# Kernel tuning notes

Hardware: AMD Instinct MI355X
Metric: run time of the kernel (lower is better)

## Reference

```python
import jax, jax.numpy as jnp
import numpy as np

B, S, E, H, F = 4, 2048, 1024, 16, 4096
D = E // H
EPS = 1e-5


def setup_inputs() -> dict:
    key = jax.random.key(0)
    ks = jax.random.split(key, 12)
    sc_e = 1.0 / np.sqrt(E)
    sc_f = 1.0 / np.sqrt(F)
    inp = {
        'x': jax.random.normal(ks[0], (B, S, E), jnp.float32),
        'mask': jnp.tril(jnp.ones((S, S), jnp.int32))[None, None],  # causal [1,1,S,S]
        'ln1_g': jnp.ones((E,), jnp.float32),
        'ln1_b': jnp.zeros((E,), jnp.float32),
        'Wq': jax.random.normal(ks[1], (E, E), jnp.float32) * sc_e,
        'bq': jnp.zeros((E,), jnp.float32),
        'Wk': jax.random.normal(ks[2], (E, E), jnp.float32) * sc_e,
        'bk': jnp.zeros((E,), jnp.float32),
        'Wv': jax.random.normal(ks[3], (E, E), jnp.float32) * sc_e,
        'bv': jnp.zeros((E,), jnp.float32),
        'Wo': jax.random.normal(ks[4], (E, E), jnp.float32) * sc_e,
        'bo': jnp.zeros((E,), jnp.float32),
        'ln2_g': jnp.ones((E,), jnp.float32),
        'ln2_b': jnp.zeros((E,), jnp.float32),
        'W1': jax.random.normal(ks[5], (F, E), jnp.float32) * sc_e,
        'b1': jnp.zeros((F,), jnp.float32),
        'W2': jax.random.normal(ks[6], (E, F), jnp.float32) * sc_f,
        'b2': jnp.zeros((E,), jnp.float32),
    }
    return inp


def _ln(x, g, b):
    m = jnp.mean(x, axis=-1, keepdims=True)
    v = jnp.mean(jnp.square(x - m), axis=-1, keepdims=True)
    return (x - m) * jax.lax.rsqrt(v + EPS) * g + b


def _attn(h, mask, Wq, bq, Wk, bk, Wv, bv, Wo, bo):
    b, s, _ = h.shape
    q = (h @ Wq.T + bq).reshape(b, s, H, D)
    k = (h @ Wk.T + bk).reshape(b, s, H, D)
    v = (h @ Wv.T + bv).reshape(b, s, H, D)
    scores = jnp.einsum('bqhd,bkhd->bhqk', q, k) / np.sqrt(D)
    scores = jnp.where(mask == 0, -jnp.inf, scores)
    w = jax.nn.softmax(scores, axis=-1)
    ctx = jnp.einsum('bhqk,bkhd->bqhd', w, v).reshape(b, s, E)
    return ctx @ Wo.T + bo


def reference(x, mask, ln1_g, ln1_b, Wq, bq, Wk, bk, Wv, bv, Wo, bo,
              ln2_g, ln2_b, W1, b1, W2, b2):
    x = x + _attn(_ln(x, ln1_g, ln1_b), mask, Wq, bq, Wk, bk, Wv, bv, Wo, bo)
    h = _ln(x, ln2_g, ln2_b)
    ffn = jax.nn.gelu(h @ W1.T + b1, approximate=False) @ W2.T + b2
    return x + ffn
```

## Files before the change

kernel.cpp:

```cpp
#include <hip/hip_runtime.h>
#include <cstdint>
#include <cstddef>

#define E_DIM 1024
#define F_DIM 4096
#define S_LEN 2048
#define NB    4
#define NH    16
#define HD    64
#define MROWS 8192

typedef __bf16 bf16x8 __attribute__((ext_vector_type(8)));
typedef float  f32x4  __attribute__((ext_vector_type(4)));

struct alignas(16) f4 { float x, y, z, w; };
__device__ __forceinline__ f4 ld4(const float* p){ return *(const f4*)p; }

__device__ __forceinline__ unsigned short f2bf(float f){
  union { float f; unsigned int u; } c; c.f = f;
  unsigned int u = c.u;
  return (unsigned short)((u + 0x7FFFu + ((u >> 16) & 1u)) >> 16);
}

__global__ void cvt_kernel(const float* __restrict__ in, unsigned short* __restrict__ out,
                           int n, float scale){
  int i = (blockIdx.x * 256 + threadIdx.x) * 4;
  if (i >= n) return;
  f4 f = ld4(in + i);
  ushort4 o;
  o.x = f2bf(f.x * scale); o.y = f2bf(f.y * scale);
  o.z = f2bf(f.z * scale); o.w = f2bf(f.w * scale);
  *(ushort4*)(out + i) = o;
}

__global__ void bias_cat(const float* __restrict__ bq, const float* __restrict__ bk,
                         const float* __restrict__ bv, float* __restrict__ out, float qsc){
  int i = blockIdx.x * 256 + threadIdx.x;
  if (i >= 3 * E_DIM) return;
  float v = (i < E_DIM) ? bq[i] * qsc : (i < 2 * E_DIM ? bk[i - E_DIM] : bv[i - 2 * E_DIM]);
  out[i] = v;
}

__global__ __launch_bounds__(256) void ln_kernel(const float* __restrict__ in,
                                                 const float* __restrict__ g,
                                                 const float* __restrict__ b,
                                                 unsigned short* __restrict__ out){
  const int row = blockIdx.x;
  const int t = threadIdx.x;
  const float* xr = in + (size_t)row * E_DIM;
  f4 xv = ld4(xr + t * 4);
  float s  = xv.x + xv.y + xv.z + xv.w;
  float ss = xv.x*xv.x + xv.y*xv.y + xv.z*xv.z + xv.w*xv.w;
  #pragma unroll
  for (int o = 1; o < 64; o <<= 1){ s += __shfl_xor(s, o); ss += __shfl_xor(ss, o); }
  __shared__ float sa[4], sb[4];
  if ((t & 63) == 0){ sa[t >> 6] = s; sb[t >> 6] = ss; }
  __syncthreads();
  s  = sa[0] + sa[1] + sa[2] + sa[3];
  ss = sb[0] + sb[1] + sb[2] + sb[3];
  const float mean = s * (1.0f / E_DIM);
  const float var  = ss * (1.0f / E_DIM) - mean * mean;
  const float rstd = rsqrtf(var + 1e-5f);
  f4 gv = ld4(g + t * 4);
  f4 bv = ld4(b + t * 4);
  ushort4 o;
  o.x = f2bf((xv.x - mean) * rstd * gv.x + bv.x);
  o.y = f2bf((xv.y - mean) * rstd * gv.y + bv.y);
  o.z = f2bf((xv.z - mean) * rstd * gv.z + bv.z);
  o.w = f2bf((xv.w - mean) * rstd * gv.w + bv.w);
  *(ushort4*)(out + (size_t)row * E_DIM + t * 4) = o;
}

__device__ __forceinline__ void async_cp16(const unsigned short* g, unsigned short* l){
  __builtin_amdgcn_global_load_lds((const __attribute__((address_space(1))) unsigned int*)g,
                                   (__attribute__((address_space(3)))       unsigned int*)l,
                                   16, 0, 0);
}

template<int EPI>
__global__ __launch_bounds__(256) void gemm_bt(const unsigned short* __restrict__ A,
                                               const unsigned short* __restrict__ W,
                                               const float* __restrict__ bias,
                                               const float* __restrict__ res,
                                               void* __restrict__ outp,
                                               int M, int N, int K){
  __shared__ unsigned short As[128 * 64];
  __shared__ unsigned short Bs[128 * 64];
  const int bn = blockIdx.x, bm = blockIdx.y;
  const int tid = threadIdx.x;
  const int wv = tid >> 6, lane = tid & 63;
  const int lr = lane & 15, qd = lane >> 4;
  const int wm = (wv >> 1) * 64, wn = (wv & 1) * 64;

  f32x4 acc[4][4];
  #pragma unroll
  for (int mt = 0; mt < 4; ++mt)
    #pragma unroll
    for (int nt = 0; nt < 4; ++nt)
      acc[mt][nt] = f32x4{0.f, 0.f, 0.f, 0.f};

  int soff[4];
  int srow[4];
  #pragma unroll
  for (int it = 0; it < 4; ++it){
    const int cc = tid + it * 256;
    srow[it] = cc >> 3;
    soff[it] = (((cc & 7) ^ (srow[it] & 7))) * 8;
  }
  const unsigned short* Abase = A + (size_t)(bm * 128) * K;
  const unsigned short* Wbase = W + (size_t)(bn * 128) * K;

  for (int k0 = 0; k0 < K; k0 += 64){
    __syncthreads();
    #pragma unroll
    for (int it = 0; it < 4; ++it){
      async_cp16(Abase + (size_t)srow[it] * K + k0 + soff[it], &As[(tid + it * 256) * 8]);
      async_cp16(Wbase + (size_t)srow[it] * K + k0 + soff[it], &Bs[(tid + it * 256) * 8]);
    }
    __builtin_amdgcn_s_waitcnt(0);
    __syncthreads();

    #pragma unroll
    for (int kk = 0; kk < 2; ++kk){
      bf16x8 af[4], bf[4];
      #pragma unroll
      for (int mt = 0; mt < 4; ++mt){
        const int fr = wm + mt * 16 + lr;
        af[mt] = *(const bf16x8*)&As[fr * 64 + (((kk * 4 + qd) ^ (fr & 7))) * 8];
      }
      #pragma unroll
      for (int nt = 0; nt < 4; ++nt){
        const int fr = wn + nt * 16 + lr;
        bf[nt] = *(const bf16x8*)&Bs[fr * 64 + (((kk * 4 + qd) ^ (fr & 7))) * 8];
      }
      #pragma unroll
      for (int mt = 0; mt < 4; ++mt)
        #pragma unroll
        for (int nt = 0; nt < 4; ++nt)
          acc[mt][nt] = __builtin_amdgcn_mfma_f32_16x16x32_bf16(af[mt], bf[nt], acc[mt][nt], 0, 0, 0);
    }
  }

  #pragma unroll
  for (int mt = 0; mt < 4; ++mt){
    #pragma unroll
    for (int r = 0; r < 4; ++r){
      const int gm = bm * 128 + wm + mt * 16 + qd * 4 + r;
      const size_t rowoff = (size_t)gm * N;
      #pragma unroll
      for (int nt = 0; nt < 4; ++nt){
        const int gn = bn * 128 + wn + nt * 16 + lr;
        float v = acc[mt][nt][r] + bias[gn];
        if constexpr (EPI == 1) v = 0.5f * v * (1.0f + erff(v * 0.70710678118654752f));
        if constexpr (EPI == 2) ((float*)outp)[rowoff + gn] = v + res[rowoff + gn];
        else                    ((unsigned short*)outp)[rowoff + gn] = f2bf(v);
      }
    }
  }
}

__global__ __launch_bounds__(256) void vtrans(const unsigned short* __restrict__ QKV,
                                              unsigned short* __restrict__ Vt){
  __shared__ unsigned short Ts[64 * 66];
  const int st = blockIdx.x;
  const int h = blockIdx.y, b = blockIdx.z;
  const int tid = threadIdx.x;
  const size_t srcbase = (size_t)(b * S_LEN + st * 64) * 3072 + 2 * E_DIM + h * HD;
  #pragma unroll
  for (int it = 0; it < 4; ++it){
    const int ch = tid + it * 256;
    const int row = ch >> 4, c4 = (ch & 15) * 4;
    *(ushort4*)&Ts[row * 66 + c4] = *(const ushort4*)(QKV + srcbase + (size_t)row * 3072 + c4);
  }
  __syncthreads();
  const size_t dstbase = (size_t)((b * NH + h) * HD) * S_LEN + st * 64;
  #pragma unroll
  for (int it = 0; it < 4; ++it){
    const int ch = tid + it * 256;
    const int d = ch >> 4, t4 = (ch & 15) * 4;
    ushort4 o;
    o.x = Ts[(t4 + 0) * 66 + d];
    o.y = Ts[(t4 + 1) * 66 + d];
    o.z = Ts[(t4 + 2) * 66 + d];
    o.w = Ts[(t4 + 3) * 66 + d];
    *(ushort4*)&Vt[dstbase + (size_t)d * S_LEN + t4] = o;
  }
}

#define AST 72
__global__ __launch_bounds__(256) void attn_mfma(const unsigned short* __restrict__ QKV,
                                                 const unsigned short* __restrict__ Vt,
                                                 unsigned short* __restrict__ Om){
  __shared__ unsigned short Ks[64 * AST];
  __shared__ unsigned short Vs[64 * AST];
  __shared__ unsigned short Ps[64 * AST];
  const int pairi = blockIdx.x;
  const int h = blockIdx.y, b = blockIdx.z;
  const int tid = threadIdx.x;
  const int w = tid >> 6, lane = tid & 63;
  const int lr = lane & 15, qd = lane >> 4;
  const size_t row0 = (size_t)b * S_LEN;
  const int qcol = h * HD;
  const int kcol = E_DIM + h * HD;
  const unsigned short* Vtb = Vt + (size_t)((b * NH + h) * HD) * S_LEN;

  bf16x8 ones;
  #pragma unroll
  for (int j = 0; j < 8; ++j) ones[j] = (__bf16)1.0f;

  for (int ph = 0; ph < 2; ++ph){
    const int qb_t = ph ? (31 - pairi) : pairi;
    const int q0 = qb_t * 64 + w * 16;

    bf16x8 qf[2];
    #pragma unroll
    for (int kk = 0; kk < 2; ++kk)
      qf[kk] = *(const bf16x8*)(QKV + (row0 + q0 + lr) * 3072 + qcol + kk * 32 + qd * 8);

    f32x4 accd[4];
    #pragma unroll
    for (int dt = 0; dt < 4; ++dt) accd[dt] = f32x4{0.f, 0.f, 0.f, 0.f};
    f32x4 lacc = f32x4{0.f, 0.f, 0.f, 0.f};

    for (int kt = 0; kt <= qb_t; ++kt){
      __syncthreads();
      #pragma unroll
      for (int it = 0; it < 2; ++it){
        const int ch = tid + it * 256;
        const int r_ = ch >> 3, c8 = (ch & 7) * 8;
        *(uint4*)&Ks[r_ * AST + c8] = *(const uint4*)(QKV + (row0 + kt * 64 + r_) * 3072 + kcol + c8);
        *(uint4*)&Vs[r_ * AST + c8] = *(const uint4*)(Vtb + (size_t)r_ * S_LEN + kt * 64 + c8);
      }
      __syncthreads();

      f32x4 s[4];
      #pragma unroll
      for (int nt = 0; nt < 4; ++nt) s[nt] = f32x4{0.f, 0.f, 0.f, 0.f};
      #pragma unroll
      for (int kk = 0; kk < 2; ++kk){
        bf16x8 kf[4];
        #pragma unroll
        for (int nt = 0; nt < 4; ++nt)
          kf[nt] = *(const bf16x8*)&Ks[(nt * 16 + lr) * AST + kk * 32 + qd * 8];
        #pragma unroll
        for (int nt = 0; nt < 4; ++nt)
          s[nt] = __builtin_amdgcn_mfma_f32_16x16x32_bf16(qf[kk], kf[nt], s[nt], 0, 0, 0);
      }
      if (kt == qb_t){
        #pragma unroll
        for (int nt = 0; nt < 4; ++nt)
          #pragma unroll
          for (int r = 0; r < 4; ++r){
            const int q  = q0 + qd * 4 + r;
            const int ky = kt * 64 + nt * 16 + lr;
            if (ky > q) s[nt][r] = -3e38f;
          }
      }
      #pragma unroll
      for (int nt = 0; nt < 4; ++nt)
        #pragma unroll
        for (int r = 0; r < 4; ++r){
          union { float f; unsigned u; } cc;
          cc.f = exp2f(s[nt][r]);
          Ps[(w * 16 + qd * 4 + r) * AST + nt * 16 + lr] = (unsigned short)((cc.u + 0x8000u) >> 16);
        }
      __builtin_amdgcn_s_waitcnt(0xc07f);
      #pragma unroll
      for (int kk = 0; kk < 2; ++kk){
        bf16x8 pf = *(const bf16x8*)&Ps[(w * 16 + lr) * AST + kk * 32 + qd * 8];
        bf16x8 vf[4];
        #pragma unroll
        for (int dt = 0; dt < 4; ++dt)
          vf[dt] = *(const bf16x8*)&Vs[(dt * 16 + lr) * AST + kk * 32 + qd * 8];
        #pragma unroll
        for (int dt = 0; dt < 4; ++dt)
          accd[dt] = __builtin_amdgcn_mfma_f32_16x16x32_bf16(pf, vf[dt], accd[dt], 0, 0, 0);
        lacc = __builtin_amdgcn_mfma_f32_16x16x32_bf16(pf, ones, lacc, 0, 0, 0);
      }
    }

    #pragma unroll
    for (int r = 0; r < 4; ++r){
      const float inv = 1.0f / lacc[r];
      const size_t ro = (row0 + q0 + qd * 4 + r) * E_DIM + qcol;
      #pragma unroll
      for (int dt = 0; dt < 4; ++dt)
        Om[ro + dt * 16 + lr] = f2bf(accd[dt][r] * inv);
    }
  }
}

extern "C" void kernel_launch(void* const* d_in, const int* in_sizes, int n_in,
                              void* d_out, int out_size, void* d_ws, size_t ws_size,
                              hipStream_t stream){
  const float* x    = (const float*)d_in[0];
  const float* ln1g = (const float*)d_in[2];
  const float* ln1b = (const float*)d_in[3];
  const float* Wq   = (const float*)d_in[4];
  const float* bq   = (const float*)d_in[5];
  const float* Wk   = (const float*)d_in[6];
  const float* bk   = (const float*)d_in[7];
  const float* Wv   = (const float*)d_in[8];
  const float* bv   = (const float*)d_in[9];
  const float* Wo   = (const float*)d_in[10];
  const float* bo   = (const float*)d_in[11];
  const float* ln2g = (const float*)d_in[12];
  const float* ln2b = (const float*)d_in[13];
  const float* W1   = (const float*)d_in[14];
  const float* b1   = (const float*)d_in[15];
  const float* W2   = (const float*)d_in[16];
  const float* b2   = (const float*)d_in[17];

  char* ws = (char*)d_ws;
  const size_t MB = 1024 * 1024;
  unsigned short* Wqkv_b = (unsigned short*)(ws + 0 * MB);
  unsigned short* Wo_b   = (unsigned short*)(ws + 6 * MB);
  unsigned short* W1_b   = (unsigned short*)(ws + 8 * MB);
  unsigned short* W2_b   = (unsigned short*)(ws + 16 * MB);
  unsigned short* qkvb   = (unsigned short*)(ws + 24 * MB);
  float*          bqkv   = (float*)(ws + 72 * MB);
  unsigned short* Vt_g   = (unsigned short*)(ws + 72 * MB);
  unsigned short* lnb    = (unsigned short*)(ws + 88 * MB);
  float*          xres   = (float*)(ws + 104 * MB);
  unsigned short* ffn1   = (unsigned short*)(ws + 24 * MB);
  unsigned short* ctxb   = lnb;

  const float QSC = 0.125f * 1.4426950408889634f;

  cvt_kernel<<<1024, 256, 0, stream>>>(Wq, Wqkv_b,                   E_DIM * E_DIM, QSC);
  cvt_kernel<<<1024, 256, 0, stream>>>(Wk, Wqkv_b + E_DIM * E_DIM,   E_DIM * E_DIM, 1.0f);
  cvt_kernel<<<1024, 256, 0, stream>>>(Wv, Wqkv_b + 2 * E_DIM * E_DIM, E_DIM * E_DIM, 1.0f);
  cvt_kernel<<<1024, 256, 0, stream>>>(Wo, Wo_b, E_DIM * E_DIM, 1.0f);
  cvt_kernel<<<4096, 256, 0, stream>>>(W1, W1_b, F_DIM * E_DIM, 1.0f);
  cvt_kernel<<<4096, 256, 0, stream>>>(W2, W2_b, F_DIM * E_DIM, 1.0f);
  bias_cat<<<12, 256, 0, stream>>>(bq, bk, bv, bqkv, QSC);

  ln_kernel<<<MROWS, 256, 0, stream>>>(x, ln1g, ln1b, lnb);

  gemm_bt<0><<<dim3(3 * E_DIM / 128, MROWS / 128), 256, 0, stream>>>(
      lnb, Wqkv_b, bqkv, nullptr, qkvb, MROWS, 3 * E_DIM, E_DIM);

  vtrans<<<dim3(S_LEN / 64, NH, NB), 256, 0, stream>>>(qkvb, Vt_g);

  attn_mfma<<<dim3(16, NH, NB), 256, 0, stream>>>(qkvb, Vt_g, ctxb);

  gemm_bt<2><<<dim3(E_DIM / 128, MROWS / 128), 256, 0, stream>>>(
      ctxb, Wo_b, bo, x, xres, MROWS, E_DIM, E_DIM);

  ln_kernel<<<MROWS, 256, 0, stream>>>(xres, ln2g, ln2b, lnb);

  gemm_bt<1><<<dim3(F_DIM / 128, MROWS / 128), 256, 0, stream>>>(
      lnb, W1_b, b1, nullptr, ffn1, MROWS, F_DIM, E_DIM);

  gemm_bt<2><<<dim3(E_DIM / 128, MROWS / 128), 256, 0, stream>>>(
      ffn1, W2_b, b2, xres, (float*)d_out, MROWS, E_DIM, F_DIM);
}
```

Measured before the change: 577.7 us.

## Add 256x256-tile 8-wave pipelined GEMM for QKV and FFN1 projections

Adds a new GEMM kernel with 256x256 output tiles, 512 threads, double-buffered async global-to-LDS copies with XOR swizzling, and interleaved quarter-tile MFMA phases with barriers and setprio. It is used for the QKV and FFN-up GEMMs in place of the 128x128 kernel, aiming to raise arithmetic intensity per LDS byte and overlap loads with MFMA work. The costs are larger LDS use (128KB per block), many barriers per K step, fewer blocks (grid of 384/512 tiles), and reliance on manual vmcnt waits being correct.

```diff
diff --git a/kernel.cpp b/kernel.cpp
--- a/kernel.cpp
+++ b/kernel.cpp
@@ -157,6 +157,143 @@
       }
     }
   }
+}
+
+#define VMW4() asm volatile("s_waitcnt vmcnt(4)" ::: "memory")
+#define VMW0() asm volatile("s_waitcnt vmcnt(0)" ::: "memory")
+#define BAR()  __builtin_amdgcn_s_barrier()
+
+template<int EPI>
+__global__ __launch_bounds__(512, 2) void gemm256(const unsigned short* __restrict__ A,
+                                                  const unsigned short* __restrict__ W,
+                                                  const float* __restrict__ bias,
+                                                  unsigned short* __restrict__ outp,
+                                                  int M, int N, int K){
+  __shared__ unsigned short lds[2][2][256 * 64];
+  const int bn = blockIdx.x, bm = blockIdx.y;
+  const int tid = threadIdx.x;
+  const int lane = tid & 63;
+  const int wv = tid >> 6;
+  const int lr = lane & 15, qd = lane >> 4;
+  const int wm = wv >> 2, wn = wv & 3;
+  const int NT = K >> 6;
+
+  f32x4 acc[2][2][4][2];
+  #pragma unroll
+  for (int a = 0; a < 2; ++a)
+    #pragma unroll
+    for (int b = 0; b < 2; ++b)
+      #pragma unroll
+      for (int c = 0; c < 4; ++c)
+        #pragma unroll
+        for (int d = 0; d < 2; ++d)
+          acc[a][b][c][d] = f32x4{0.f, 0.f, 0.f, 0.f};
+
+  const int srow = tid >> 3;
+  const int scol = ((tid & 7) ^ (srow & 7)) * 8;
+  const unsigned short* Ab = A + (size_t)(bm * 256 + srow) * K + scol;
+  const unsigned short* Wb = W + (size_t)(bn * 256 + srow) * K + scol;
+
+#define STAGE_A(bufi, h, kt) do{ \
+    async_cp16(Ab + (size_t)((h)*128     ) * K + (size_t)(kt) * 64, &lds[bufi][0][((h)*128     ) * 64 + tid * 8]); \
+    async_cp16(Ab + (size_t)((h)*128 + 64) * K + (size_t)(kt) * 64, &lds[bufi][0][((h)*128 + 64) * 64 + tid * 8]); \
+  }while(0)
+#define STAGE_B(bufi, h, kt) do{ \
+    async_cp16(Wb + (size_t)((h)*128     ) * K + (size_t)(kt) * 64, &lds[bufi][1][((h)*128     ) * 64 + tid * 8]); \
+    async_cp16(Wb + (size_t)((h)*128 + 64) * K + (size_t)(kt) * 64, &lds[bufi][1][((h)*128 + 64) * 64 + tid * 8]); \
+  }while(0)
+
+  const int sw0 = ((qd    ) ^ (lr & 7)) * 8;
+  const int sw1 = ((qd + 4) ^ (lr & 7)) * 8;
+  const int arow = wm * 64 + lr;
+  const int brow = wn * 32 + lr;
+
+  bf16x8 af[4][2], b0[2][2], b1[2][2];
+
+#define LDA(bufi, mh) do{ \
+    _Pragma("unroll") \
+    for (int mt = 0; mt < 4; ++mt){ \
+      const int r_ = (mh)*128 + arow + mt * 16; \
+      af[mt][0] = *(const bf16x8*)&lds[bufi][0][r_ * 64 + sw0]; \
+      af[mt][1] = *(const bf16x8*)&lds[bufi][0][r_ * 64 + sw1]; \
+    } }while(0)
+#define LDB(bufi, nh, dst) do{ \
+    _Pragma("unroll") \
+    for (int nt = 0; nt < 2; ++nt){ \
+      const int r_ = (nh)*128 + brow + nt * 16; \
+      dst[nt][0] = *(const bf16x8*)&lds[bufi][1][r_ * 64 + sw0]; \
+      dst[nt][1] = *(const bf16x8*)&lds[bufi][1][r_ * 64 + sw1]; \
+    } }while(0)
+#define MMA(mh, nh, bfr) do{ \
+    __builtin_amdgcn_s_setprio(1); \
+    _Pragma("unroll") \
+    for (int kk = 0; kk < 2; ++kk) \
+      _Pragma("unroll") \
+      for (int mt = 0; mt < 4; ++mt) \
+        _Pragma("unroll") \
+        for (int nt = 0; nt < 2; ++nt) \
+          acc[mh][nh][mt][nt] = __builtin_amdgcn_mfma_f32_16x16x32_bf16(af[mt][kk], bfr[nt][kk], acc[mh][nh][mt][nt], 0, 0, 0); \
+    __builtin_amdgcn_s_setprio(0); \
+  }while(0)
+
+  STAGE_A(0, 0, 0); STAGE_B(0, 1, 0); STAGE_A(0, 1, 0); STAGE_B(0, 0, 0);
+  STAGE_A(1, 0, 1); STAGE_B(1, 1, 1);
+  VMW4(); BAR();
+
+  for (int t = 0; t < NT; t += 2){
+    const bool s2 = (t + 2) < NT, s3 = (t + 3) < NT;
+    LDA(0, 0); LDB(0, 0, b0);
+    STAGE_A(1, 1, t + 1);
+    BAR(); MMA(0, 0, b0); BAR();
+    LDB(0, 1, b1);
+    STAGE_B(1, 0, t + 1);
+    BAR(); MMA(0, 1, b1); BAR();
+    LDA(0, 1);
+    if (s2) STAGE_A(0, 0, t + 2);
+    BAR(); MMA(1, 1, b1); BAR();
+    if (s2) STAGE_B(0, 1, t + 2);
+    BAR(); MMA(1, 0, b0);
+    if (s2) { VMW4(); } else { VMW0(); }
+    BAR();
+    LDA(1, 0); LDB(1, 0, b0);
+    if (s2) STAGE_A(0, 1, t + 2);
+    BAR(); MMA(0, 0, b0); BAR();
+    LDB(1, 1, b1);
+    if (s2) STAGE_B(0, 0, t + 2);
+    BAR(); MMA(0, 1, b1); BAR();
+    LDA(1, 1);
+    if (s3) STAGE_A(1, 0, t + 3);
+    BAR(); MMA(1, 1, b1); BAR();
+    if (s3) STAGE_B(1, 1, t + 3);
+    BAR(); MMA(1, 0, b0);
+    VMW4();
+    BAR();
+  }
+
+  #pragma unroll
+  for (int mh = 0; mh < 2; ++mh)
+    #pragma unroll
+    for (int nh = 0; nh < 2; ++nh)
+      #pragma unroll
+      for (int mt = 0; mt < 4; ++mt){
+        const int gm0 = bm * 256 + mh * 128 + wm * 64 + mt * 16 + qd * 4;
+        #pragma unroll
+        for (int r = 0; r < 4; ++r){
+          const size_t rowoff = (size_t)(gm0 + r) * N;
+          #pragma unroll
+          for (int nt = 0; nt < 2; ++nt){
+            const int gn = bn * 256 + nh * 128 + wn * 32 + nt * 16 + lr;
+            float v = acc[mh][nh][mt][nt][r] + bias[gn];
+            if constexpr (EPI == 1) v = 0.5f * v * (1.0f + erff(v * 0.70710678118654752f));
+            outp[rowoff + gn] = f2bf(v);
+          }
+        }
+      }
+#undef STAGE_A
+#undef STAGE_B
+#undef LDA
+#undef LDB
+#undef MMA
 }
 
 __global__ __launch_bounds__(256) void vtrans(const unsigned short* __restrict__ QKV,
@@ -337,8 +474,8 @@
 
   ln_kernel<<<MROWS, 256, 0, stream>>>(x, ln1g, ln1b, lnb);
 
-  gemm_bt<0><<<dim3(3 * E_DIM / 128, MROWS / 128), 256, 0, stream>>>(
-      lnb, Wqkv_b, bqkv, nullptr, qkvb, MROWS, 3 * E_DIM, E_DIM);
+  gemm256<0><<<dim3(3 * E_DIM / 256, MROWS / 256), 512, 0, stream>>>(
+      lnb, Wqkv_b, bqkv, qkvb, MROWS, 3 * E_DIM, E_DIM);
 
   vtrans<<<dim3(S_LEN / 64, NH, NB), 256, 0, stream>>>(qkvb, Vt_g);
 
@@ -349,8 +486,8 @@
 
   ln_kernel<<<MROWS, 256, 0, stream>>>(xres, ln2g, ln2b, lnb);
 
-  gemm_bt<1><<<dim3(F_DIM / 128, MROWS / 128), 256, 0, stream>>>(
-      lnb, W1_b, b1, nullptr, ffn1, MROWS, F_DIM, E_DIM);
+  gemm256<1><<<dim3(F_DIM / 256, MROWS / 256), 512, 0, stream>>>(
+      lnb, W1_b, b1, ffn1, MROWS, F_DIM, E_DIM);
 
   gemm_bt<2><<<dim3(E_DIM / 128, MROWS / 128), 256, 0, stream>>>(
       ffn1, W2_b, b2, xres, (float*)d_out, MROWS, E_DIM, F_DIM);
```

Result: faster. 556.4 us (-3.7%).
